# Optimization experiments

Hardware: AMD Instinct MI355X
Metric: run time of the kernel (lower is better)

The kernel has to match this reference:

```python
import jax, jax.numpy as jnp
import numpy as np

N = 100000   # n_entity
D = 128      # kg_emb_dim
R = 12       # n_relation
NB = 8       # num_bases
E = 1_000_000
P = 400_000  # hypergraph incidences
HE = 20_000  # hyperedges
B = 64       # users in batch
LR = 64      # related entities per hypergraph per user
LC = 32      # context entities per user
NH = 8       # mha heads
HD = D // NH


def setup_inputs() -> dict:
    key = jax.random.key(0)
    ks = jax.random.split(key, 32)
    s = 1.0 / np.sqrt(D)
    f = lambda i, shape, sc=s: jax.random.normal(ks[i], shape, dtype=jnp.float32) * sc
    ri = lambda i, shape, hi: jax.random.randint(ks[i], shape, 0, hi, dtype=jnp.int32)
    return {
        'entity_emb': f(0, (N, D)),
        'rgcn_bases': f(1, (NB, D, D)),
        'rgcn_comp': f(2, (R, NB)),
        'rgcn_root': f(3, (D, D)),
        'rgcn_bias': jnp.zeros((D,), jnp.float32),
        'sess_theta': f(4, (D, D)),
        'sess_bias': jnp.zeros((D,), jnp.float32),
        'know_theta': f(5, (D, D)),
        'know_bias': jnp.zeros((D,), jnp.float32),
        'in_proj_w': f(6, (3 * D, D)),
        'in_proj_b': jnp.zeros((3 * D,), jnp.float32),
        'out_proj_w': f(7, (D, D)),
        'out_proj_b': jnp.zeros((D,), jnp.float32),
        'attn_his_a': f(8, (D, D)),
        'attn_his_b': f(9, (D, 1)),
        'attn_a': f(10, (D, D)),
        'attn_b': f(11, (D, 1)),
        'rec_bias': jnp.zeros((N,), jnp.float32),
        'edge_src': ri(12, (E,), N),
        'edge_dst': ri(13, (E,), N),
        'edge_type': ri(14, (E,), R),
        'sess_nodes': ri(15, (P,), N),
        'sess_edges': ri(16, (P,), HE),
        'know_nodes': ri(17, (P,), N),
        'know_edges': ri(18, (P,), HE),
        'sess_rel_idx': ri(19, (B, LR), N),
        'know_rel_idx': ri(20, (B, LR), N),
        'context_idx': ri(21, (B, LC), N),
    }


def rgcn_conv(x, bases, comp, root, bias, src, dst, etype):
    # PyG RGCNConv with basis decomposition; per-relation mean aggregation
    # norm = 1/|N_r(i)| : count edges per (dst, relation)
    pair_key = dst * R + etype
    cnt = jax.ops.segment_sum(jnp.ones_like(src, dtype=x.dtype), pair_key, N * R)
    norm = 1.0 / jnp.maximum(cnt[pair_key], 1.0)  # [E]
    w = jnp.einsum('rb,bio->rio', comp, bases)    # [R, D, D]
    out = x @ root + bias
    for r in range(R):
        h_r = x @ w[r]                                            # [N, D]
        coef = norm * (etype == r).astype(x.dtype)                # [E]
        out = out + jax.ops.segment_sum(h_r[src] * coef[:, None], dst, N)
    return out


def hypergraph_conv(x, theta, bias, nodes, edges, n_hyperedges):
    # PyG HypergraphConv (no attention): D^-1 H W B^-1 H^T X Theta + bias
    xt = x @ theta                                                # [N, D]
    ones = jnp.ones(nodes.shape, x.dtype)
    b_deg = jax.ops.segment_sum(ones, edges, n_hyperedges)        # [HE]
    edge_feat = jax.ops.segment_sum(xt[nodes], edges, n_hyperedges)
    edge_feat = edge_feat * jnp.where(b_deg > 0, 1.0 / b_deg, 0.0)[:, None]
    d_deg = jax.ops.segment_sum(ones, nodes, N)                   # [N]
    out = jax.ops.segment_sum(edge_feat[edges], nodes, N)
    return out * jnp.where(d_deg > 0, 1.0 / d_deg, 0.0)[:, None] + bias


def self_attn_batch(h, a, b):
    # SelfAttentionBatch: e = tanh(h a) b; softmax over nodes; weighted sum
    e = jnp.einsum('bld,dk->blk', jnp.tanh(jnp.einsum('bld,de->ble', h, a)), b)[..., 0]
    attn = jax.nn.softmax(e, axis=-1)                             # [B, L]
    return jnp.einsum('bl,bld->bd', attn, h)


def mha(q, kv, in_proj_w, in_proj_b, out_proj_w, out_proj_b):
    # torch.nn.MultiheadAttention (batch_first) math
    wq, wk, wv = in_proj_w[:D], in_proj_w[D:2 * D], in_proj_w[2 * D:]
    bq, bk, bv = in_proj_b[:D], in_proj_b[D:2 * D], in_proj_b[2 * D:]
    qh = (q @ wq.T + bq).reshape(q.shape[0], q.shape[1], NH, HD)
    kh = (kv @ wk.T + bk).reshape(kv.shape[0], kv.shape[1], NH, HD)
    vh = (kv @ wv.T + bv).reshape(kv.shape[0], kv.shape[1], NH, HD)
    logits = jnp.einsum('bqhd,bkhd->bhqk', qh, kh) / np.sqrt(HD)
    attn = jax.nn.softmax(logits, axis=-1)
    o = jnp.einsum('bhqk,bkhd->bqhd', attn, vh).reshape(q.shape[0], q.shape[1], D)
    return o @ out_proj_w.T + out_proj_b


def reference(entity_emb, rgcn_bases, rgcn_comp, rgcn_root, rgcn_bias,
              sess_theta, sess_bias, know_theta, know_bias,
              in_proj_w, in_proj_b, out_proj_w, out_proj_b,
              attn_his_a, attn_his_b, attn_a, attn_b, rec_bias,
              edge_src, edge_dst, edge_type,
              sess_nodes, sess_edges, know_nodes, know_edges,
              sess_rel_idx, know_rel_idx, context_idx):
    # 1) RGCN over the full KG
    kg = rgcn_conv(entity_emb, rgcn_bases, rgcn_comp, rgcn_root, rgcn_bias,
                   edge_src, edge_dst, edge_type)
    # 2) session / knowledge hypergraph convolutions on RGCN output
    sess = hypergraph_conv(kg, sess_theta, sess_bias, sess_nodes, sess_edges, HE)
    know = hypergraph_conv(kg, know_theta, know_bias, know_nodes, know_edges, HE)
    # 3) per-user: related = concat(session_emb, knowledge_emb); context from kg
    related = jnp.concatenate([sess[sess_rel_idx], know[know_rel_idx]], axis=1)  # [B, 2LR, D]
    context = kg[context_idx]                                                    # [B, LC, D]
    # 4) MHItemAttention (context queries related) + gated attention pooling
    att_rel = mha(context, related, in_proj_w, in_proj_b, out_proj_w, out_proj_b)
    his = self_attn_batch(att_rel, attn_his_a, attn_his_b)                       # [B, D]
    user_cat = jnp.concatenate([context, his[:, None, :]], axis=1)               # [B, LC+1, D]
    user = self_attn_batch(user_cat, attn_a, attn_b)                             # [B, D]
    # 5) recommendation scores: F.linear(user, kg_embedding, rec_bias.bias)
    return user @ kg.T + rec_bias                                                # [B, N]
```

## Files before the change

kernel.cpp:

```cpp
#include <hip/hip_runtime.h>
#include <hip/hip_bf16.h>

#define DN 100000
#define DD 128
#define DR 12
#define DNB 8
#define DE 1000000
#define DP 400000
#define DHE 20000
#define DHE2 40000
#define DB 64
#define DLR 64
#define DLC 32
#define DNH 8
#define DHD 16
#define NRBINS (DR * DN)
#define SCAN_CHUNK 1024
#define MCAP 65536

typedef unsigned short ushortT;
typedef unsigned int uintT;
typedef __attribute__((ext_vector_type(8))) short s8v;
typedef __attribute__((ext_vector_type(4))) float f4v;

#define APAD 136

__device__ __forceinline__ ushortT rneb(float v) {
    uintT b = __float_as_uint(v);
    return (ushortT)((b + 0x7FFFu + ((b >> 16) & 1u)) >> 16);
}
__device__ __forceinline__ float b2f(ushortT h) {
    return __uint_as_float(((uintT)h) << 16);
}

__device__ __forceinline__ void split_store8(ushortT* hbase, ushortT* lbase, const float* v)
{
    ushortT h[8], l[8];
    #pragma unroll
    for (int j = 0; j < 8; ++j) {
        h[j] = rneb(v[j]);
        l[j] = rneb(v[j] - b2f(h[j]));
    }
    uint4 hv = make_uint4((uintT)h[0] | ((uintT)h[1] << 16), (uintT)h[2] | ((uintT)h[3] << 16),
                          (uintT)h[4] | ((uintT)h[5] << 16), (uintT)h[6] | ((uintT)h[7] << 16));
    uint4 lv = make_uint4((uintT)l[0] | ((uintT)l[1] << 16), (uintT)l[2] | ((uintT)l[3] << 16),
                          (uintT)l[4] | ((uintT)l[5] << 16), (uintT)l[6] | ((uintT)l[7] << 16));
    *(uint4*)hbase = hv;
    *(uint4*)lbase = lv;
}


__global__ __launch_bounds__(256) void k_presplit_all(
    const float* __restrict__ root, const float* __restrict__ st,
    const float* __restrict__ kt, const float* __restrict__ ipw,
    const float* __restrict__ opw, const float* __restrict__ aha,
    const float* __restrict__ aa, ushortT* __restrict__ outA)
{
    int gid = blockIdx.x * 256 + threadIdx.x;
    int mat = gid >> 14, e = gid & 16383;
    const float* srcs[9] = {root, st, kt, ipw, ipw + 16384, ipw + 32768, opw, aha, aa};
    const float* W = srcs[mat];
    bool t1 = (mat >= 3 && mat <= 6);
    int k = e & 31, n = (e >> 5) & 127, kc = e >> 12;
    float f = t1 ? W[(size_t)n * 128 + kc * 32 + k] : W[(size_t)(kc * 32 + k) * 128 + n];
    ushortT h = rneb(f);
    outA[(size_t)mat * 32768 + e] = h;
    outA[(size_t)mat * 32768 + 16384 + e] = rneb(f - b2f(h));
}

__global__ void k_wcomp_split(const float* __restrict__ comp, const float* __restrict__ bases,
                              ushortT* __restrict__ warena)
{
    int i = blockIdx.x * blockDim.x + threadIdx.x;
    if (i >= DR * DD * DD) return;
    int r = i / (DD * DD), io = i % (DD * DD);
    float s = 0.f;
    #pragma unroll
    for (int b = 0; b < DNB; ++b) s += comp[r * DNB + b] * bases[(size_t)b * DD * DD + io];
    int irow = io >> 7, o = io & 127;
    int kc = irow >> 5, k = irow & 31;
    size_t dst = (size_t)r * 32768 + (size_t)kc * 4096 + o * 32 + k;
    ushortT h = rneb(s);
    warena[dst] = h;
    warena[dst + 16384] = rneb(s - b2f(h));
}

__global__ __launch_bounds__(256) void k_gemm_ds(
    const float* __restrict__ A, const ushortT* __restrict__ Wb,
    const float* __restrict__ bias, const float* __restrict__ rs,
    float* __restrict__ C, int M)
{
    __shared__ __align__(16) ushortT Ah[64 * APAD], Al[64 * APAD];
    __shared__ __align__(16) ushortT Bs[8192];
    int tid = threadIdx.x;
    int row0 = blockIdx.x * 64;
    {
        int row = tid >> 2, c0 = (tid & 3) * 32;
        int gr = row0 + row;
        const float* ar = A + (size_t)gr * 128 + c0;
        float sc = 1.0f;
        if (rs && gr < M) { float d = rs[gr]; sc = (d > 0.f) ? 1.0f / d : 0.f; }
        #pragma unroll
        for (int g = 0; g < 4; ++g) {
            float v[8] = {};
            if (gr < M) {
                float4 u0 = *(const float4*)(ar + g * 8);
                float4 u1 = *(const float4*)(ar + g * 8 + 4);
                v[0]=u0.x*sc; v[1]=u0.y*sc; v[2]=u0.z*sc; v[3]=u0.w*sc;
                v[4]=u1.x*sc; v[5]=u1.y*sc; v[6]=u1.z*sc; v[7]=u1.w*sc;
            }
            split_store8(&Ah[row * APAD + c0 + g * 8], &Al[row * APAD + c0 + g * 8], v);
        }
    }
    f4v acc[8] = {};
    int w = tid >> 6, lane = tid & 63, m = lane & 15, quad = lane >> 4;
    for (int kc = 0; kc < 4; ++kc) {
        __syncthreads();
        {
            const ushortT* gh = Wb + kc * 4096;
            const ushortT* gl = Wb + 16384 + kc * 4096;
            *(s8v*)&Bs[tid * 8]        = *(const s8v*)&gh[tid * 8];
            *(s8v*)&Bs[2048 + tid * 8] = *(const s8v*)&gh[2048 + tid * 8];
            *(s8v*)&Bs[4096 + tid * 8] = *(const s8v*)&gl[tid * 8];
            *(s8v*)&Bs[6144 + tid * 8] = *(const s8v*)&gl[2048 + tid * 8];
        }
        __syncthreads();
        s8v ah = *(const s8v*)&Ah[(w * 16 + m) * APAD + kc * 32 + quad * 8];
        s8v al = *(const s8v*)&Al[(w * 16 + m) * APAD + kc * 32 + quad * 8];
        #pragma unroll
        for (int nt = 0; nt < 8; ++nt) {
            int boff = (nt * 16 + m) * 32 + quad * 8;
            s8v bh = *(const s8v*)&Bs[boff];
            s8v bl = *(const s8v*)&Bs[4096 + boff];
            acc[nt] = __builtin_amdgcn_mfma_f32_16x16x32_bf16(ah, bh, acc[nt], 0, 0, 0);
            acc[nt] = __builtin_amdgcn_mfma_f32_16x16x32_bf16(al, bh, acc[nt], 0, 0, 0);
            acc[nt] = __builtin_amdgcn_mfma_f32_16x16x32_bf16(ah, bl, acc[nt], 0, 0, 0);
        }
    }
    float bv[8];
    #pragma unroll
    for (int nt = 0; nt < 8; ++nt) bv[nt] = bias ? bias[nt * 16 + m] : 0.f;
    #pragma unroll
    for (int rr = 0; rr < 4; ++rr) {
        int gr = row0 + w * 16 + quad * 4 + rr;
        if (gr < M) {
            #pragma unroll
            for (int nt = 0; nt < 8; ++nt)
                C[(size_t)gr * 128 + nt * 16 + m] = acc[nt][rr] + bv[nt];
        }
    }
}

__global__ __launch_bounds__(256) void k_tanh_dot_ds(
    const float* __restrict__ A, const ushortT* __restrict__ Wb,
    const float* __restrict__ bvec, float* __restrict__ e, int M)
{
    __shared__ __align__(16) ushortT Ah[64 * APAD], Al[64 * APAD];
    __shared__ __align__(16) ushortT Bs[8192];
    int tid = threadIdx.x;
    int row0 = blockIdx.x * 64;
    {
        int row = tid >> 2, c0 = (tid & 3) * 32;
        int gr = row0 + row;
        const float* ar = A + (size_t)gr * 128 + c0;
        #pragma unroll
        for (int g = 0; g < 4; ++g) {
            float v[8] = {};
            if (gr < M) {
                float4 u0 = *(const float4*)(ar + g * 8);
                float4 u1 = *(const float4*)(ar + g * 8 + 4);
                v[0]=u0.x; v[1]=u0.y; v[2]=u0.z; v[3]=u0.w;
                v[4]=u1.x; v[5]=u1.y; v[6]=u1.z; v[7]=u1.w;
            }
            split_store8(&Ah[row * APAD + c0 + g * 8], &Al[row * APAD + c0 + g * 8], v);
        }
    }
    f4v acc[8] = {};
    int w = tid >> 6, lane = tid & 63, m = lane & 15, quad = lane >> 4;
    for (int kc = 0; kc < 4; ++kc) {
        __syncthreads();
        {
            const ushortT* gh = Wb + kc * 4096;
            const ushortT* gl = Wb + 16384 + kc * 4096;
            *(s8v*)&Bs[tid * 8]        = *(const s8v*)&gh[tid * 8];
            *(s8v*)&Bs[2048 + tid * 8] = *(const s8v*)&gh[2048 + tid * 8];
            *(s8v*)&Bs[4096 + tid * 8] = *(const s8v*)&gl[tid * 8];
            *(s8v*)&Bs[6144 + tid * 8] = *(const s8v*)&gl[2048 + tid * 8];
        }
        __syncthreads();
        s8v ah = *(const s8v*)&Ah[(w * 16 + m) * APAD + kc * 32 + quad * 8];
        s8v al = *(const s8v*)&Al[(w * 16 + m) * APAD + kc * 32 + quad * 8];
        #pragma unroll
        for (int nt = 0; nt < 8; ++nt) {
            int boff = (nt * 16 + m) * 32 + quad * 8;
            s8v bh = *(const s8v*)&Bs[boff];
            s8v bl = *(const s8v*)&Bs[4096 + boff];
            acc[nt] = __builtin_amdgcn_mfma_f32_16x16x32_bf16(ah, bh, acc[nt], 0, 0, 0);
            acc[nt] = __builtin_amdgcn_mfma_f32_16x16x32_bf16(al, bh, acc[nt], 0, 0, 0);
            acc[nt] = __builtin_amdgcn_mfma_f32_16x16x32_bf16(ah, bl, acc[nt], 0, 0, 0);
        }
    }
    float bv[8];
    #pragma unroll
    for (int nt = 0; nt < 8; ++nt) bv[nt] = bvec[nt * 16 + m];
    #pragma unroll
    for (int rr = 0; rr < 4; ++rr) {
        float p = 0.f;
        #pragma unroll
        for (int nt = 0; nt < 8; ++nt) p += tanhf(acc[nt][rr]) * bv[nt];
        #pragma unroll
        for (int o = 1; o < 16; o <<= 1) p += __shfl_xor(p, o);
        int gr = row0 + w * 16 + quad * 4 + rr;
        if (m == 0 && gr < M) e[gr] = p;
    }
}

template <int L>
__global__ __launch_bounds__(128) void k_pool_apply(const float* __restrict__ h,
                                                    const float* __restrict__ e,
                                                    float* __restrict__ out,
                                                    ushortT* __restrict__ us)
{
    __shared__ float es[L];
    int b = blockIdx.x, tid = threadIdx.x;
    if (tid < L) es[tid] = e[b * L + tid];
    __syncthreads();
    float mx = -1e30f;
    #pragma unroll
    for (int l = 0; l < L; ++l) mx = fmaxf(mx, es[l]);
    float wgt[L];
    float sum = 0.f;
    #pragma unroll
    for (int l = 0; l < L; ++l) { wgt[l] = __expf(es[l] - mx); sum += wgt[l]; }
    float inv = 1.0f / sum;
    float o = 0.f;
    #pragma unroll
    for (int l = 0; l < L; ++l) o += wgt[l] * h[((size_t)b * L + l) * 128 + tid];
    float val = o * inv;
    out[(size_t)b * 128 + tid] = val;
    if (us) {
        ushortT hh = rneb(val);
        ushortT ll = rneb(val - b2f(hh));
        int e_ = ((tid >> 5) * 2048) + b * 32 + (tid & 31);
        us[e_] = hh;
        us[8192 + e_] = ll;
    }
}

__global__ void k_build_ucat(const float* __restrict__ ctx, const float* __restrict__ his,
                             float* ucat)
{
    int i = blockIdx.x * blockDim.x + threadIdx.x;
    if (i >= DB * 33 * 128) return;
    int d = i & 127, l = (i >> 7) % 33, b = i / (33 * 128);
    ucat[i] = (l < 32) ? ctx[((size_t)b * 32 + l) * 128 + d] : his[(size_t)b * 128 + d];
}

__global__ __launch_bounds__(256) void k_rgcn_ds(
    const float* __restrict__ x, const ushortT* __restrict__ warena,
    const int* __restrict__ seglist, const int* __restrict__ soff,
    const int* __restrict__ slen, const int* __restrict__ ssrc,
    const int* __restrict__ stypebase, float* __restrict__ kg, int r)
{
    __shared__ __align__(16) ushortT Ah[64 * APAD], Al[64 * APAD];
    __shared__ __align__(16) ushortT Bs[8192];
    int s0 = stypebase[r], s1 = stypebase[r + 1];
    int base = s0 + blockIdx.x * 64;
    if (base >= s1) return;
    int nrow = min(64, s1 - base);
    int tid = threadIdx.x;
    const ushortT* Wb = warena + (size_t)r * 32768;
    {
        int row = tid >> 2, c0 = (tid & 3) * 32;
        float a[32] = {};
        if (row < nrow) {
            int key = seglist[base + row];
            int st = soff[key], len = slen[key];
            for (int i = 0; i < len; ++i) {
                const float* xr = x + (size_t)ssrc[st + i] * 128 + c0;
                #pragma unroll
                for (int j = 0; j < 8; ++j) {
                    float4 v = *(const float4*)(xr + j * 4);
                    a[j*4+0] += v.x; a[j*4+1] += v.y; a[j*4+2] += v.z; a[j*4+3] += v.w;
                }
            }
            float inv = 1.0f / (float)max(len, 1);
            #pragma unroll
            for (int j = 0; j < 32; ++j) a[j] *= inv;
        }
        #pragma unroll
        for (int g = 0; g < 4; ++g)
            split_store8(&Ah[row * APAD + c0 + g * 8], &Al[row * APAD + c0 + g * 8], a + g * 8);
    }
    f4v acc[8] = {};
    int w = tid >> 6, lane = tid & 63, m = lane & 15, quad = lane >> 4;
    for (int kc = 0; kc < 4; ++kc) {
        __syncthreads();
        {
            const ushortT* gh = Wb + kc * 4096;
            const ushortT* gl = Wb + 16384 + kc * 4096;
            *(s8v*)&Bs[tid * 8]        = *(const s8v*)&gh[tid * 8];
            *(s8v*)&Bs[2048 + tid * 8] = *(const s8v*)&gh[2048 + tid * 8];
            *(s8v*)&Bs[4096 + tid * 8] = *(const s8v*)&gl[tid * 8];
            *(s8v*)&Bs[6144 + tid * 8] = *(const s8v*)&gl[2048 + tid * 8];
        }
        __syncthreads();
        s8v ah = *(const s8v*)&Ah[(w * 16 + m) * APAD + kc * 32 + quad * 8];
        s8v al = *(const s8v*)&Al[(w * 16 + m) * APAD + kc * 32 + quad * 8];
        #pragma unroll
        for (int nt = 0; nt < 8; ++nt) {
            int boff = (nt * 16 + m) * 32 + quad * 8;
            s8v bh = *(const s8v*)&Bs[boff];
            s8v bl = *(const s8v*)&Bs[4096 + boff];
            acc[nt] = __builtin_amdgcn_mfma_f32_16x16x32_bf16(ah, bh, acc[nt], 0, 0, 0);
            acc[nt] = __builtin_amdgcn_mfma_f32_16x16x32_bf16(al, bh, acc[nt], 0, 0, 0);
            acc[nt] = __builtin_amdgcn_mfma_f32_16x16x32_bf16(ah, bl, acc[nt], 0, 0, 0);
        }
    }
    #pragma unroll
    for (int rr = 0; rr < 4; ++rr) {
        int rt = w * 16 + quad * 4 + rr;
        if (rt < nrow) {
            int dst = seglist[base + rt] - r * DN;
            float* kr = kg + (size_t)dst * 128 + m;
            #pragma unroll
            for (int nt = 0; nt < 8; ++nt)
                kr[nt * 16] += acc[nt][rr];
        }
    }
}

__global__ __launch_bounds__(256) void k_score_ds(
    const float* __restrict__ kg, const ushortT* __restrict__ Ub,
    const float* __restrict__ rb, float* __restrict__ out)
{
    __shared__ __align__(16) ushortT Ah[64 * APAD], Al[64 * APAD];
    __shared__ __align__(16) ushortT Bs[4096];
    int tid = threadIdx.x;
    int n0 = blockIdx.x * 64;
    {
        int row = tid >> 2, c0 = (tid & 3) * 32;
        int gr = n0 + row;
        const float* ar = kg + (size_t)gr * 128 + c0;
        #pragma unroll
        for (int g = 0; g < 4; ++g) {
            float v[8] = {};
            if (gr < DN) {
                float4 u0 = *(const float4*)(ar + g * 8);
                float4 u1 = *(const float4*)(ar + g * 8 + 4);
                v[0]=u0.x; v[1]=u0.y; v[2]=u0.z; v[3]=u0.w;
                v[4]=u1.x; v[5]=u1.y; v[6]=u1.z; v[7]=u1.w;
            }
            split_store8(&Ah[row * APAD + c0 + g * 8], &Al[row * APAD + c0 + g * 8], v);
        }
    }
    f4v acc[4] = {};
    int w = tid >> 6, lane = tid & 63, m = lane & 15, quad = lane >> 4;
    for (int kc = 0; kc < 4; ++kc) {
        __syncthreads();
        {
            const ushortT* gh = Ub + kc * 2048;
            const ushortT* gl = Ub + 8192 + kc * 2048;
            *(s8v*)&Bs[tid * 8]        = *(const s8v*)&gh[tid * 8];
            *(s8v*)&Bs[2048 + tid * 8] = *(const s8v*)&gl[tid * 8];
        }
        __syncthreads();
        s8v ah = *(const s8v*)&Ah[(w * 16 + m) * APAD + kc * 32 + quad * 8];
        s8v al = *(const s8v*)&Al[(w * 16 + m) * APAD + kc * 32 + quad * 8];
        #pragma unroll
        for (int nt = 0; nt < 4; ++nt) {
            int boff = (nt * 16 + m) * 32 + quad * 8;
            s8v bh = *(const s8v*)&Bs[boff];
            s8v bl = *(const s8v*)&Bs[2048 + boff];
            acc[nt] = __builtin_amdgcn_mfma_f32_16x16x32_bf16(ah, bh, acc[nt], 0, 0, 0);
            acc[nt] = __builtin_amdgcn_mfma_f32_16x16x32_bf16(al, bh, acc[nt], 0, 0, 0);
            acc[nt] = __builtin_amdgcn_mfma_f32_16x16x32_bf16(ah, bl, acc[nt], 0, 0, 0);
        }
    }
    int n = n0 + w * 16 + quad * 4;
    if (n < DN) {
        float4 rbv = *(const float4*)&rb[n];
        #pragma unroll
        for (int nt = 0; nt < 4; ++nt) {
            int b = nt * 16 + m;
            float4 o = make_float4(acc[nt][0] + rbv.x, acc[nt][1] + rbv.y,
                                   acc[nt][2] + rbv.z, acc[nt][3] + rbv.w);
            *(float4*)&out[(size_t)b * DN + n] = o;
        }
    }
}

__global__ void k_scan_pass1(const int* __restrict__ in, int n, int* __restrict__ bsum)
{
    __shared__ int red[256];
    int b = blockIdx.x, t = threadIdx.x;
    int i0 = b * SCAN_CHUNK + t * 4;
    int s = 0;
    #pragma unroll
    for (int j = 0; j < 4; ++j) {
        int i = i0 + j;
        if (i < n) s += in[i];
    }
    red[t] = s;
    __syncthreads();
    for (int o = 128; o > 0; o >>= 1) {
        if (t < o) red[t] += red[t + o];
        __syncthreads();
    }
    if (t == 0) bsum[b] = red[0];
}

__global__ __launch_bounds__(256) void k_scan_pass2p(int* bsum, int nb, int* total)
{
    __shared__ int lds[256];
    __shared__ int carry;
    int t = threadIdx.x;
    if (t == 0) carry = 0;
    __syncthreads();
    for (int c0 = 0; c0 < nb; c0 += 256) {
        int i = c0 + t;
        int v = (i < nb) ? bsum[i] : 0;
        lds[t] = v;
        __syncthreads();
        for (int o = 1; o < 256; o <<= 1) {
            int add = (t >= o) ? lds[t - o] : 0;
            __syncthreads();
            lds[t] += add;
            __syncthreads();
        }
        int myc = carry;
        if (i < nb) bsum[i] = lds[t] - v + myc;
        int tot = lds[255];
        __syncthreads();
        if (t == 0) carry = myc + tot;
        __syncthreads();
    }
    if (total && t == 0) *total = carry;
}

__global__ void k_scan_pass3(const int* __restrict__ in, int n, const int* __restrict__ bsum,
                             int* __restrict__ out)
{
    __shared__ int lds[256];
    int b = blockIdx.x, t = threadIdx.x;
    int i0 = b * SCAN_CHUNK + t * 4;
    int v[4]; int s = 0;
    #pragma unroll
    for (int j = 0; j < 4; ++j) {
        int i = i0 + j;
        int x = 0;
        if (i < n) x = in[i];
        v[j] = x; s += x;
    }
    lds[t] = s;
    __syncthreads();
    for (int o = 1; o < 256; o <<= 1) {
        int add = (t >= o) ? lds[t - o] : 0;
        __syncthreads();
        lds[t] += add;
        __syncthreads();
    }
    int run = lds[t] - s + bsum[b];
    #pragma unroll
    for (int j = 0; j < 4; ++j) {
        int i = i0 + j;
        if (i < n) { out[i] = run; run += v[j]; }
    }
}

__global__ void k_scan2_pass1(const int* __restrict__ in, int n, int* bV, int* bP)
{
    __shared__ int redV[256], redP[256];
    int b = blockIdx.x, t = threadIdx.x;
    int i0 = b * SCAN_CHUNK + t * 4;
    int sv = 0, sp = 0;
    #pragma unroll
    for (int j = 0; j < 4; ++j) {
        int i = i0 + j;
        if (i < n) { int v = in[i]; sv += v; sp += (v > 0); }
    }
    redV[t] = sv; redP[t] = sp;
    __syncthreads();
    for (int o = 128; o > 0; o >>= 1) {
        if (t < o) { redV[t] += redV[t + o]; redP[t] += redP[t + o]; }
        __syncthreads();
    }
    if (t == 0) { bV[b] = redV[0]; bP[b] = redP[0]; }
}

__global__ __launch_bounds__(256) void k_scan2_pass2(int* bV, int* bP, int nb, int* totalP)
{
    __shared__ int lds[256];
    __shared__ int carry;
    int t = threadIdx.x;
    #pragma unroll 1
    for (int which = 0; which < 2; ++which) {
        int* bsum = which ? bP : bV;
        __syncthreads();
        if (t == 0) carry = 0;
        __syncthreads();
        for (int c0 = 0; c0 < nb; c0 += 256) {
            int i = c0 + t;
            int v = (i < nb) ? bsum[i] : 0;
            lds[t] = v;
            __syncthreads();
            for (int o = 1; o < 256; o <<= 1) {
                int add = (t >= o) ? lds[t - o] : 0;
                __syncthreads();
                lds[t] += add;
                __syncthreads();
            }
            int myc = carry;
            if (i < nb) bsum[i] = lds[t] - v + myc;
            int tot = lds[255];
            __syncthreads();
            if (t == 0) carry = myc + tot;
            __syncthreads();
        }
        if (which == 1 && totalP && t == 0) *totalP = carry;
    }
}

__global__ void k_scan2_pass3(const int* __restrict__ in, int n,
                              const int* __restrict__ bV, const int* __restrict__ bP,
                              int* __restrict__ outV, int* __restrict__ outP)
{
    __shared__ int ldsV[256], ldsP[256];
    int b = blockIdx.x, t = threadIdx.x;
    int i0 = b * SCAN_CHUNK + t * 4;
    int v[4]; int sv = 0, sp = 0;
    #pragma unroll
    for (int j = 0; j < 4; ++j) {
        int i = i0 + j;
        int x = 0;
        if (i < n) x = in[i];
        v[j] = x; sv += x; sp += (x > 0);
    }
    ldsV[t] = sv; ldsP[t] = sp;
    __syncthreads();
    for (int o = 1; o < 256; o <<= 1) {
        int addV = (t >= o) ? ldsV[t - o] : 0;
        int addP = (t >= o) ? ldsP[t - o] : 0;
        __syncthreads();
        ldsV[t] += addV; ldsP[t] += addP;
        __syncthreads();
    }
    int runV = ldsV[t] - sv + bV[b];
    int runP = ldsP[t] - sp + bP[b];
    #pragma unroll
    for (int j = 0; j < 4; ++j) {
        int i = i0 + j;
        if (i < n) {
            outV[i] = runV; outP[i] = runP;
            runV += v[j]; runP += (v[j] > 0);
        }
    }
}

__global__ void k_hist_rgcn(const int* __restrict__ dst, const int* __restrict__ et,
                            int* hist, int E)
{
    int i = blockIdx.x * blockDim.x + threadIdx.x;
    if (i < E) atomicAdd(&hist[(size_t)et[i] * DN + dst[i]], 1);
}

__global__ void k_seglist(const int* __restrict__ hist, const int* __restrict__ segpos,
                          int* __restrict__ seglist, int n)
{
    int i = blockIdx.x * blockDim.x + threadIdx.x;
    if (i < n && hist[i] > 0) seglist[segpos[i]] = i;
}

__global__ void k_stypebase(const int* __restrict__ segpos, int* stypebase)
{
    int t = threadIdx.x;
    if (t < DR) stypebase[t] = segpos[(size_t)t * DN];
}

__global__ void k_bucket_rgcn(const int* __restrict__ src, const int* __restrict__ dst,
                              const int* __restrict__ et, const int* __restrict__ off,
                              int* cur, int* ssrc, int E)
{
    int i = blockIdx.x * blockDim.x + threadIdx.x;
    if (i >= E) return;
    int key = et[i] * DN + dst[i];
    int pos = off[key] + atomicAdd(&cur[key], 1);
    ssrc[pos] = src[i];
}

__global__ void k_hist_p2(const int* __restrict__ se, const int* __restrict__ ke, int* hist)
{
    int i = blockIdx.x * blockDim.x + threadIdx.x;
    if (i < DP) atomicAdd(&hist[se[i]], 1);
    else if (i < 2 * DP) atomicAdd(&hist[DHE + ke[i - DP]], 1);
}

__global__ void k_bucket_p2(const int* __restrict__ sn, const int* __restrict__ se,
                            const int* __restrict__ kn, const int* __restrict__ ke,
                            const int* __restrict__ off, int* cur, int* pns)
{
    int i = blockIdx.x * blockDim.x + threadIdx.x;
    if (i >= 2 * DP) return;
    int e, node;
    if (i < DP) { e = se[i]; node = sn[i]; }
    else { e = DHE + ke[i - DP]; node = kn[i - DP]; }
    int pos = off[e] + atomicAdd(&cur[e], 1);
    pns[pos] = node;
}

__global__ void k_hyper_agg(const float* __restrict__ xsrc, const int* __restrict__ pns,
                            const int* __restrict__ hoff, const int* __restrict__ hcnt,
                            const int* __restrict__ heneed, float* __restrict__ efeat)
{
    int lane = threadIdx.x & 63;
    int he = (blockIdx.x * blockDim.x + threadIdx.x) >> 6;
    if (he >= DHE2) return;
    if (!heneed[he]) return;
    int st = hoff[he], len = hcnt[he];
    int half = lane >> 5;
    int c16 = (lane & 31) * 4;
    float4 acc = make_float4(0.f, 0.f, 0.f, 0.f);
    int c = 0;
    for (; c + 4 <= len; c += 4) {
        int n0 = pns[st + c + half];
        int n1 = pns[st + c + 2 + half];
        float4 v0 = *(const float4*)&xsrc[(size_t)n0 * 128 + c16];
        float4 v1 = *(const float4*)&xsrc[(size_t)n1 * 128 + c16];
        acc.x += v0.x + v1.x; acc.y += v0.y + v1.y;
        acc.z += v0.z + v1.z; acc.w += v0.w + v1.w;
    }
    for (; c < len; c += 2) {
        int idx = c + half;
        if (idx < len) {
            int n = pns[st + idx];
            float4 v = *(const float4*)&xsrc[(size_t)n * 128 + c16];
            acc.x += v.x; acc.y += v.y; acc.z += v.z; acc.w += v.w;
        }
    }
    acc.x += __shfl_xor(acc.x, 32);
    acc.y += __shfl_xor(acc.y, 32);
    acc.z += __shfl_xor(acc.z, 32);
    acc.w += __shfl_xor(acc.w, 32);
    if (half == 0) {
        float inv = (len > 0) ? 1.0f / (float)len : 0.f;
        float4 o = make_float4(acc.x * inv, acc.y * inv, acc.z * inv, acc.w * inv);
        *(float4*)&efeat[(size_t)he * 128 + c16] = o;
    }
}

__global__ void k_slot_assign2(const int* __restrict__ sidx, const int* __restrict__ kidx,
                               int* slot_s, int* slot_k, int* scnt)
{
    int i = blockIdx.x * blockDim.x + threadIdx.x;
    if (i < DB * DLR) {
        int node = sidx[i];
        if (atomicCAS(&slot_s[node], -1, -2) == -1) slot_s[node] = atomicAdd(&scnt[0], 1);
    } else if (i < 2 * DB * DLR) {
        int node = kidx[i - DB * DLR];
        if (atomicCAS(&slot_k[node], -1, -2) == -1) slot_k[node] = atomicAdd(&scnt[1], 1);
    }
}

__global__ __launch_bounds__(256) void k_sdeg_match(
    const int* __restrict__ nodes, const int* __restrict__ he, const int* __restrict__ slot,
    float* sdeg, int* mcnt, int* mhe, int* msl, int* heneed, int heBase)
{
    __shared__ int lcnt, lbase;
    if (threadIdx.x == 0) lcnt = 0;
    __syncthreads();
    int i = blockIdx.x * 256 + threadIdx.x;
    int s = -1, lidx = 0, h = 0;
    if (i < DP) {
        s = slot[nodes[i]];
        if (s >= 0) {
            h = heBase + he[i];
            heneed[h] = 1;
            atomicAdd(&sdeg[s], 1.0f);
            lidx = atomicAdd(&lcnt, 1);
        }
    }
    __syncthreads();
    if (threadIdx.x == 0) lbase = (lcnt > 0) ? atomicAdd(mcnt, lcnt) : 0;
    __syncthreads();
    if (s >= 0) {
        int idx = lbase + lidx;
        if (idx < MCAP) { mhe[idx] = h; msl[idx] = s; }
    }
}

__global__ void k_accmatch2(const float* __restrict__ efeat,
                            const int* __restrict__ mhe_s, const int* __restrict__ msl_s,
                            const int* __restrict__ mhe_k, const int* __restrict__ msl_k,
                            const int* __restrict__ mcnt,
                            float* sacc_s, float* sacc_k)
{
    int lane = threadIdx.x & 63;
    int w = (blockIdx.x * blockDim.x + threadIdx.x) >> 6;
    int nw = (gridDim.x * blockDim.x) >> 6;
    int Ms = min(mcnt[0], MCAP), Mk = min(mcnt[1], MCAP);
    for (int i = w; i < Ms + Mk; i += nw) {
        bool sess = i < Ms;
        int he = sess ? mhe_s[i] : mhe_k[i - Ms];
        int sl = sess ? msl_s[i] : msl_k[i - Ms];
        float* sacc = sess ? sacc_s : sacc_k;
        float2 v = *(const float2*)&efeat[(size_t)he * 128 + lane * 2];
        atomicAdd(&sacc[(size_t)sl * 128 + lane * 2],     v.x);
        atomicAdd(&sacc[(size_t)sl * 128 + lane * 2 + 1], v.y);
    }
}

__global__ void k_rel_gather2(const float* __restrict__ so_s, const float* __restrict__ so_k,
                              const int* __restrict__ slot_s, const int* __restrict__ slot_k,
                              const int* __restrict__ ridx_s, const int* __restrict__ ridx_k,
                              float* __restrict__ related)
{
    int gid = blockIdx.x * blockDim.x + threadIdx.x;
    int i = gid >> 5, c = gid & 31;
    if (i >= 2 * DB * DLR) return;
    bool sess = i < DB * DLR;
    int ii = sess ? i : i - DB * DLR;
    int s = sess ? slot_s[ridx_s[ii]] : slot_k[ridx_k[ii]];
    const float* so = sess ? so_s : so_k;
    int b = ii / DLR, l = ii % DLR;
    int colOff = sess ? 0 : 64;
    ((float4*)&related[((size_t)b * 128 + colOff + l) * 128])[c] =
        ((const float4*)&so[(size_t)s * 128])[c];
}

__global__ void k_gather_rows(const float* __restrict__ src, const int* __restrict__ idx,
                              float* dst, int nRows)
{
    int i = blockIdx.x * blockDim.x + threadIdx.x;
    if (i >= nRows * 128) return;
    int row = i >> 7, d = i & 127;
    dst[i] = src[(size_t)idx[row] * 128 + d];
}

__global__ __launch_bounds__(256) void k_mha(const float* __restrict__ qb,
                                             const float* __restrict__ kb,
                                             const float* __restrict__ vb,
                                             float* __restrict__ ob)
{
    int b = blockIdx.x >> 3, h = blockIdx.x & 7;
    __shared__ float Ks[128][16], Vs[128][16], Qs[32][16];
    int tid = threadIdx.x;
    for (int i = tid; i < 128 * 16; i += 256) {
        int j = i >> 4, d = i & 15;
        Ks[j][d] = kb[((size_t)b * 128 + j) * 128 + h * 16 + d];
        Vs[j][d] = vb[((size_t)b * 128 + j) * 128 + h * 16 + d];
    }
    for (int i = tid; i < 32 * 16; i += 256) {
        int q = i >> 4, d = i & 15;
        Qs[q][d] = qb[((size_t)b * 32 + q) * 128 + h * 16 + d] * 0.25f;
    }
    __syncthreads();
    int q = tid >> 3;
    int jg = tid & 7;
    float lg[16];
    float m = -1e30f;
    #pragma unroll
    for (int jj = 0; jj < 16; ++jj) {
        int j = jg * 16 + jj;
        float s = 0.f;
        #pragma unroll
        for (int d = 0; d < 16; ++d) s += Qs[q][d] * Ks[j][d];
        lg[jj] = s;
        m = fmaxf(m, s);
    }
    #pragma unroll
    for (int o = 1; o < 8; o <<= 1) m = fmaxf(m, __shfl_xor(m, o));
    float sum = 0.f;
    float acc[16] = {};
    #pragma unroll
    for (int jj = 0; jj < 16; ++jj) {
        float p = __expf(lg[jj] - m);
        sum += p;
        int j = jg * 16 + jj;
        #pragma unroll
        for (int d = 0; d < 16; ++d) acc[d] += p * Vs[j][d];
    }
    #pragma unroll
    for (int o = 1; o < 8; o <<= 1) {
        sum += __shfl_xor(sum, o);
        #pragma unroll
        for (int d = 0; d < 16; ++d) acc[d] += __shfl_xor(acc[d], o);
    }
    if (jg == 0) {
        float inv = 1.0f / sum;
        #pragma unroll
        for (int d = 0; d < 16; ++d)
            ob[((size_t)b * 32 + q) * 128 + h * 16 + d] = acc[d] * inv;
    }
}

extern "C" void kernel_launch(void* const* d_in, const int* in_sizes, int n_in,
                              void* d_out, int out_size, void* d_ws, size_t ws_size,
                              hipStream_t stream)
{
    const float* emb        = (const float*)d_in[0];
    const float* bases      = (const float*)d_in[1];
    const float* comp       = (const float*)d_in[2];
    const float* root       = (const float*)d_in[3];
    const float* rgcn_bias  = (const float*)d_in[4];
    const float* sess_theta = (const float*)d_in[5];
    const float* sess_bias  = (const float*)d_in[6];
    const float* know_theta = (const float*)d_in[7];
    const float* know_bias  = (const float*)d_in[8];
    const float* in_proj_w  = (const float*)d_in[9];
    const float* in_proj_b  = (const float*)d_in[10];
    const float* out_proj_w = (const float*)d_in[11];
    const float* out_proj_b = (const float*)d_in[12];
    const float* attn_his_a = (const float*)d_in[13];
    const float* attn_his_b = (const float*)d_in[14];
    const float* attn_a     = (const float*)d_in[15];
    const float* attn_b     = (const float*)d_in[16];
    const float* rec_bias   = (const float*)d_in[17];
    const int* edge_src     = (const int*)d_in[18];
    const int* edge_dst     = (const int*)d_in[19];
    const int* edge_type    = (const int*)d_in[20];
    const int* sess_nodes   = (const int*)d_in[21];
    const int* sess_edges   = (const int*)d_in[22];
    const int* know_nodes   = (const int*)d_in[23];
    const int* know_edges   = (const int*)d_in[24];
    const int* sess_rel_idx = (const int*)d_in[25];
    const int* know_rel_idx = (const int*)d_in[26];
    const int* context_idx  = (const int*)d_in[27];
    float* out = (float*)d_out;

    float* wsf = (float*)d_ws;
    size_t off = 0;
    auto alloc = [&](size_t n) { size_t r = off; off += (n + 255) & ~(size_t)255; return r; };
    float* kg      = wsf + alloc(12800000);
    float* tmp     = wsf + alloc(12800000);
    ushortT* warena = (ushortT*)(wsf + alloc(196608));
    int*   bsumV   = (int*)(wsf + alloc(2048));
    int*   bsumP   = (int*)(wsf + alloc(2048));
    int*   stybase = (int*)(wsf + alloc(16));
    size_t zstart = off;
    int*   hhist   = (int*)(wsf + alloc(DHE2));
    int*   hcur    = (int*)(wsf + alloc(DHE2));
    int*   heneed  = (int*)(wsf + alloc(DHE2));
    int*   mcnt    = (int*)(wsf + alloc(16));
    int*   scnt    = (int*)(wsf + alloc(16));
    float* sdeg_s  = wsf + alloc(4096);
    float* sdeg_k  = wsf + alloc(4096);
    float* sacc_s  = wsf + alloc(524288);
    float* sacc_k  = wsf + alloc(524288);
    size_t zend = off;
    size_t fstart = off;
    int*   slot_s  = (int*)(wsf + alloc(100000));
    int*   slot_k  = (int*)(wsf + alloc(100000));
    size_t fend = off;
    int*   hoff    = (int*)(wsf + alloc(DHE2));
    int*   pns     = (int*)(wsf + alloc(2 * DP));
    int*   mhe_s   = (int*)(wsf + alloc(MCAP));
    int*   msl_s   = (int*)(wsf + alloc(MCAP));
    int*   mhe_k   = (int*)(wsf + alloc(MCAP));
    int*   msl_k   = (int*)(wsf + alloc(MCAP));
    float* so_s    = wsf + alloc(524288);
    float* so_k    = wsf + alloc(524288);
    float* related = wsf + alloc(1048576);
    float* ctx     = wsf + alloc(262144);
    float* qb      = wsf + alloc(262144);
    float* kb      = wsf + alloc(1048576);
    float* vb      = wsf + alloc(1048576);
    float* obuf    = wsf + alloc(262144);
    float* attrel  = wsf + alloc(262144);
    float* his     = wsf + alloc(8192);
    float* ucat    = wsf + alloc(270336);
    float* userb   = wsf + alloc(8192);
    float* e1      = wsf + alloc(2048);
    float* e2      = wsf + alloc(2112);
    (void)ws_size; (void)in_sizes; (void)n_in; (void)out_size;

    int*   hist    = (int*)tmp;
    int*   rcur    = (int*)tmp + 1200000;
    int*   soff    = (int*)tmp + 2400000;
    int*   segpos  = (int*)tmp + 3600000;
    int*   seglist = (int*)tmp + 4800000;
    int*   ssrc    = (int*)tmp + 6000000;
    float* efeat   = tmp + 7000000;
    ushortT* wsplit = (ushortT*)(tmp + 12200000);
    ushortT* usplit = (ushortT*)(tmp + 12400000);

    const int nbR = (NRBINS + SCAN_CHUNK - 1) / SCAN_CHUNK;
    const int nbH = (DHE2 + SCAN_CHUNK - 1) / SCAN_CHUNK;

    hipMemsetAsync(wsf + zstart, 0, (zend - zstart) * 4, stream);
    hipMemsetAsync(wsf + fstart, 0xFF, (fend - fstart) * 4, stream);
    hipMemsetAsync(hist, 0, 2400000 * 4, stream);

    k_presplit_all<<<576, 256, 0, stream>>>(root, sess_theta, know_theta, in_proj_w,
                                            out_proj_w, attn_his_a, attn_a, wsplit);

    k_slot_assign2<<<32, 256, 0, stream>>>(sess_rel_idx, know_rel_idx, slot_s, slot_k, scnt);
    k_sdeg_match<<<(DP + 255) / 256, 256, 0, stream>>>(sess_nodes, sess_edges, slot_s,
                                                       sdeg_s, mcnt, mhe_s, msl_s, heneed, 0);
    k_sdeg_match<<<(DP + 255) / 256, 256, 0, stream>>>(know_nodes, know_edges, slot_k,
                                                       sdeg_k, mcnt + 1, mhe_k, msl_k, heneed, DHE);

    k_hist_rgcn<<<(DE + 255) / 256, 256, 0, stream>>>(edge_dst, edge_type, hist, DE);
    k_scan2_pass1<<<nbR, 256, 0, stream>>>(hist, NRBINS, bsumV, bsumP);
    k_scan2_pass2<<<1, 256, 0, stream>>>(bsumV, bsumP, nbR, stybase + DR);
    k_scan2_pass3<<<nbR, 256, 0, stream>>>(hist, NRBINS, bsumV, bsumP, soff, segpos);
    k_stypebase<<<1, 64, 0, stream>>>(segpos, stybase);
    k_seglist<<<(NRBINS + 255) / 256, 256, 0, stream>>>(hist, segpos, seglist, NRBINS);
    k_bucket_rgcn<<<(DE + 255) / 256, 256, 0, stream>>>(edge_src, edge_dst, edge_type,
                                                        soff, rcur, ssrc, DE);
    k_wcomp_split<<<(DR * DD * DD + 255) / 256, 256, 0, stream>>>(comp, bases, warena);

    int gemmN = (DN + 63) / 64;
    k_gemm_ds<<<gemmN, 256, 0, stream>>>(emb, wsplit + 0 * 32768, rgcn_bias, nullptr, kg, DN);
    for (int r = 0; r < DR; ++r)
        k_rgcn_ds<<<gemmN, 256, 0, stream>>>(emb, warena, seglist, soff, hist, ssrc,
                                             stybase, kg, r);

    k_hist_p2<<<(2 * DP + 255) / 256, 256, 0, stream>>>(sess_edges, know_edges, hhist);
    k_scan_pass1<<<nbH, 256, 0, stream>>>(hhist, DHE2, bsumV);
    k_scan_pass2p<<<1, 256, 0, stream>>>(bsumV, nbH, nullptr);
    k_scan_pass3<<<nbH, 256, 0, stream>>>(hhist, DHE2, bsumV, hoff);
    k_bucket_p2<<<(2 * DP + 255) / 256, 256, 0, stream>>>(sess_nodes, sess_edges,
                                                          know_nodes, know_edges,
                                                          hoff, hcur, pns);
    k_hyper_agg<<<(DHE2 * 64 + 255) / 256, 256, 0, stream>>>(kg, pns, hoff, hhist, heneed, efeat);
    k_accmatch2<<<256, 256, 0, stream>>>(efeat, mhe_s, msl_s, mhe_k, msl_k, mcnt, sacc_s, sacc_k);

    k_gemm_ds<<<64, 256, 0, stream>>>(sacc_s, wsplit + 1 * 32768, sess_bias, sdeg_s, so_s, 4096);
    k_gemm_ds<<<64, 256, 0, stream>>>(sacc_k, wsplit + 2 * 32768, know_bias, sdeg_k, so_k, 4096);
    k_rel_gather2<<<(2 * DB * DLR * 32 + 255) / 256, 256, 0, stream>>>(
        so_s, so_k, slot_s, slot_k, sess_rel_idx, know_rel_idx, related);

    k_gather_rows<<<(DB * DLC * 128 + 255) / 256, 256, 0, stream>>>(kg, context_idx, ctx, DB * DLC);
    k_gemm_ds<<<(DB * DLC + 63) / 64, 256, 0, stream>>>(ctx, wsplit + 3 * 32768,
                                                        in_proj_b, nullptr, qb, DB * DLC);
    k_gemm_ds<<<(DB * 128 + 63) / 64, 256, 0, stream>>>(related, wsplit + 4 * 32768,
                                                        in_proj_b + DD, nullptr, kb, DB * 128);
    k_gemm_ds<<<(DB * 128 + 63) / 64, 256, 0, stream>>>(related, wsplit + 5 * 32768,
                                                        in_proj_b + 2 * DD, nullptr, vb, DB * 128);
    k_mha<<<DB * DNH, 256, 0, stream>>>(qb, kb, vb, obuf);
    k_gemm_ds<<<(DB * DLC + 63) / 64, 256, 0, stream>>>(obuf, wsplit + 6 * 32768,
                                                        out_proj_b, nullptr, attrel, DB * DLC);

    k_tanh_dot_ds<<<(DB * DLC + 63) / 64, 256, 0, stream>>>(attrel, wsplit + 7 * 32768,
                                                            attn_his_b, e1, DB * DLC);
    k_pool_apply<32><<<DB, 128, 0, stream>>>(attrel, e1, his, nullptr);
    k_build_ucat<<<(DB * 33 * 128 + 255) / 256, 256, 0, stream>>>(ctx, his, ucat);
    k_tanh_dot_ds<<<(DB * 33 + 63) / 64, 256, 0, stream>>>(ucat, wsplit + 8 * 32768,
                                                           attn_b, e2, DB * 33);
    k_pool_apply<33><<<DB, 128, 0, stream>>>(ucat, e2, userb, usplit);
    k_score_ds<<<gemmN, 256, 0, stream>>>(kg, usplit, rec_bias, out);
}
```

Baseline: 985.3 us.

## Merge per-relation RGCN launches into one kernel and fuse histogram/bucket passes

Replaces the 12 per-relation RGCN launches, each sized for all nodes with most blocks exiting early, with a single launch. A prefix table maps each block to its relation, and because blocks from different relations may now hit the same destination row concurrently, the output update becomes an atomicAdd. The RGCN and hypergraph histogram and bucketing kernels are merged. Bucketing now increments the scan offsets in place, which removes the cursor arrays, and readers subtract the length to recover the segment start. The context row gather is folded into the Q-projection GEMM, which also writes the gathered rows out. The cost is float atomics on kg, which make the summation order nondeterministic.

```diff
diff --git a/kernel.cpp b/kernel.cpp
--- a/kernel.cpp
+++ b/kernel.cpp
@@ -49,7 +49,6 @@
     *(uint4*)lbase = lv;
 }
 
-
 __global__ __launch_bounds__(256) void k_presplit_all(
     const float* __restrict__ root, const float* __restrict__ st,
     const float* __restrict__ kt, const float* __restrict__ ipw,
@@ -88,6 +87,7 @@
 __global__ __launch_bounds__(256) void k_gemm_ds(
     const float* __restrict__ A, const ushortT* __restrict__ Wb,
     const float* __restrict__ bias, const float* __restrict__ rs,
+    const int* __restrict__ gidx, float* __restrict__ gout,
     float* __restrict__ C, int M)
 {
     __shared__ __align__(16) ushortT Ah[64 * APAD], Al[64 * APAD];
@@ -97,7 +97,9 @@
     {
         int row = tid >> 2, c0 = (tid & 3) * 32;
         int gr = row0 + row;
-        const float* ar = A + (size_t)gr * 128 + c0;
+        int arow = gr;
+        if (gidx && gr < M) arow = gidx[gr];
+        const float* ar = A + (size_t)arow * 128 + c0;
         float sc = 1.0f;
         if (rs && gr < M) { float d = rs[gr]; sc = (d > 0.f) ? 1.0f / d : 0.f; }
         #pragma unroll
@@ -108,6 +110,10 @@
                 float4 u1 = *(const float4*)(ar + g * 8 + 4);
                 v[0]=u0.x*sc; v[1]=u0.y*sc; v[2]=u0.z*sc; v[3]=u0.w*sc;
                 v[4]=u1.x*sc; v[5]=u1.y*sc; v[6]=u1.z*sc; v[7]=u1.w*sc;
+                if (gout) {
+                    *(float4*)(gout + (size_t)gr * 128 + c0 + g * 8)     = u0;
+                    *(float4*)(gout + (size_t)gr * 128 + c0 + g * 8 + 4) = u1;
+                }
             }
             split_store8(&Ah[row * APAD + c0 + g * 8], &Al[row * APAD + c0 + g * 8], v);
         }
@@ -256,17 +262,22 @@
     ucat[i] = (l < 32) ? ctx[((size_t)b * 32 + l) * 128 + d] : his[(size_t)b * 128 + d];
 }
 
-__global__ __launch_bounds__(256) void k_rgcn_ds(
+__global__ __launch_bounds__(256) void k_rgcn_all(
     const float* __restrict__ x, const ushortT* __restrict__ warena,
     const int* __restrict__ seglist, const int* __restrict__ soff,
     const int* __restrict__ slen, const int* __restrict__ ssrc,
-    const int* __restrict__ stypebase, float* __restrict__ kg, int r)
+    const int* __restrict__ stypebase, const int* __restrict__ bo,
+    float* __restrict__ kg)
 {
     __shared__ __align__(16) ushortT Ah[64 * APAD], Al[64 * APAD];
     __shared__ __align__(16) ushortT Bs[8192];
+    int bid = blockIdx.x;
+    if (bid >= bo[DR]) return;
+    int r = 0;
+    #pragma unroll 1
+    while (bid >= bo[r + 1]) ++r;
     int s0 = stypebase[r], s1 = stypebase[r + 1];
-    int base = s0 + blockIdx.x * 64;
-    if (base >= s1) return;
+    int base = s0 + (bid - bo[r]) * 64;
     int nrow = min(64, s1 - base);
     int tid = threadIdx.x;
     const ushortT* Wb = warena + (size_t)r * 32768;
@@ -275,7 +286,8 @@
         float a[32] = {};
         if (row < nrow) {
             int key = seglist[base + row];
-            int st = soff[key], len = slen[key];
+            int len = slen[key];
+            int st = soff[key] - len;
             for (int i = 0; i < len; ++i) {
                 const float* xr = x + (size_t)ssrc[st + i] * 128 + c0;
                 #pragma unroll
@@ -325,7 +337,7 @@
             float* kr = kg + (size_t)dst * 128 + m;
             #pragma unroll
             for (int nt = 0; nt < 8; ++nt)
-                kr[nt * 16] += acc[nt][rr];
+                atomicAdd(&kr[nt * 16], acc[nt][rr]);
         }
     }
 }
@@ -557,11 +569,19 @@
     }
 }
 
-__global__ void k_hist_rgcn(const int* __restrict__ dst, const int* __restrict__ et,
-                            int* hist, int E)
+__global__ void k_hist_both(const int* __restrict__ dst, const int* __restrict__ et,
+                            int* __restrict__ hist,
+                            const int* __restrict__ se, const int* __restrict__ ke,
+                            int* __restrict__ hhist)
 {
     int i = blockIdx.x * blockDim.x + threadIdx.x;
-    if (i < E) atomicAdd(&hist[(size_t)et[i] * DN + dst[i]], 1);
+    if (i < DE) {
+        atomicAdd(&hist[(size_t)et[i] * DN + dst[i]], 1);
+    } else {
+        int j = i - DE;
+        if (j < DP) atomicAdd(&hhist[se[j]], 1);
+        else if (j < 2 * DP) atomicAdd(&hhist[DHE + ke[j - DP]], 1);
+    }
 }
 
 __global__ void k_seglist(const int* __restrict__ hist, const int* __restrict__ segpos,
@@ -571,41 +591,43 @@
     if (i < n && hist[i] > 0) seglist[segpos[i]] = i;
 }
 
-__global__ void k_stypebase(const int* __restrict__ segpos, int* stypebase)
+__global__ void k_stypebase(const int* __restrict__ segpos, int* stybase, int* bo)
 {
     int t = threadIdx.x;
-    if (t < DR) stypebase[t] = segpos[(size_t)t * DN];
-}
-
-__global__ void k_bucket_rgcn(const int* __restrict__ src, const int* __restrict__ dst,
-                              const int* __restrict__ et, const int* __restrict__ off,
-                              int* cur, int* ssrc, int E)
+    if (t < DR) stybase[t] = segpos[(size_t)t * DN];
+    if (t == 0) {
+        int acc = 0; bo[0] = 0;
+        int prev = segpos[0];
+        for (int r = 0; r < DR; ++r) {
+            int nxt = (r == DR - 1) ? stybase[DR] : segpos[(size_t)(r + 1) * DN];
+            acc += (nxt - prev + 63) >> 6;
+            bo[r + 1] = acc;
+            prev = nxt;
+        }
+    }
+}
+
+__global__ void k_bucket_both(const int* __restrict__ src, const int* __restrict__ dst,
+                              const int* __restrict__ et, int* __restrict__ soff,
+                              int* __restrict__ ssrc,
+                              const int* __restrict__ sn, const int* __restrict__ se,
+                              const int* __restrict__ kn, const int* __restrict__ ke,
+                              int* __restrict__ hoff, int* __restrict__ pns)
 {
     int i = blockIdx.x * blockDim.x + threadIdx.x;
-    if (i >= E) return;
-    int key = et[i] * DN + dst[i];
-    int pos = off[key] + atomicAdd(&cur[key], 1);
-    ssrc[pos] = src[i];
-}
-
-__global__ void k_hist_p2(const int* __restrict__ se, const int* __restrict__ ke, int* hist)
-{
-    int i = blockIdx.x * blockDim.x + threadIdx.x;
-    if (i < DP) atomicAdd(&hist[se[i]], 1);
-    else if (i < 2 * DP) atomicAdd(&hist[DHE + ke[i - DP]], 1);
-}
-
-__global__ void k_bucket_p2(const int* __restrict__ sn, const int* __restrict__ se,
-                            const int* __restrict__ kn, const int* __restrict__ ke,
-                            const int* __restrict__ off, int* cur, int* pns)
-{
-    int i = blockIdx.x * blockDim.x + threadIdx.x;
-    if (i >= 2 * DP) return;
-    int e, node;
-    if (i < DP) { e = se[i]; node = sn[i]; }
-    else { e = DHE + ke[i - DP]; node = kn[i - DP]; }
-    int pos = off[e] + atomicAdd(&cur[e], 1);
-    pns[pos] = node;
+    if (i < DE) {
+        int key = et[i] * DN + dst[i];
+        int pos = atomicAdd(&soff[key], 1);
+        ssrc[pos] = src[i];
+    } else {
+        int j = i - DE;
+        if (j >= 2 * DP) return;
+        int e, node;
+        if (j < DP) { e = se[j]; node = sn[j]; }
+        else { e = DHE + ke[j - DP]; node = kn[j - DP]; }
+        int pos = atomicAdd(&hoff[e], 1);
+        pns[pos] = node;
+    }
 }
 
 __global__ void k_hyper_agg(const float* __restrict__ xsrc, const int* __restrict__ pns,
@@ -616,7 +638,8 @@
     int he = (blockIdx.x * blockDim.x + threadIdx.x) >> 6;
     if (he >= DHE2) return;
     if (!heneed[he]) return;
-    int st = hoff[he], len = hcnt[he];
+    int len = hcnt[he];
+    int st = hoff[he] - len;
     int half = lane >> 5;
     int c16 = (lane & 31) * 4;
     float4 acc = make_float4(0.f, 0.f, 0.f, 0.f);
@@ -725,15 +748,6 @@
     int colOff = sess ? 0 : 64;
     ((float4*)&related[((size_t)b * 128 + colOff + l) * 128])[c] =
         ((const float4*)&so[(size_t)s * 128])[c];
-}
-
-__global__ void k_gather_rows(const float* __restrict__ src, const int* __restrict__ idx,
-                              float* dst, int nRows)
-{
-    int i = blockIdx.x * blockDim.x + threadIdx.x;
-    if (i >= nRows * 128) return;
-    int row = i >> 7, d = i & 127;
-    dst[i] = src[(size_t)idx[row] * 128 + d];
 }
 
 __global__ __launch_bounds__(256) void k_mha(const float* __restrict__ qb,
@@ -836,9 +850,9 @@
     int*   bsumV   = (int*)(wsf + alloc(2048));
     int*   bsumP   = (int*)(wsf + alloc(2048));
     int*   stybase = (int*)(wsf + alloc(16));
+    int*   bo      = (int*)(wsf + alloc(16));
     size_t zstart = off;
     int*   hhist   = (int*)(wsf + alloc(DHE2));
-    int*   hcur    = (int*)(wsf + alloc(DHE2));
     int*   heneed  = (int*)(wsf + alloc(DHE2));
     int*   mcnt    = (int*)(wsf + alloc(16));
     int*   scnt    = (int*)(wsf + alloc(16));
@@ -874,12 +888,11 @@
     (void)ws_size; (void)in_sizes; (void)n_in; (void)out_size;
 
     int*   hist    = (int*)tmp;
-    int*   rcur    = (int*)tmp + 1200000;
-    int*   soff    = (int*)tmp + 2400000;
-    int*   segpos  = (int*)tmp + 3600000;
-    int*   seglist = (int*)tmp + 4800000;
-    int*   ssrc    = (int*)tmp + 6000000;
-    float* efeat   = tmp + 7000000;
+    int*   soff    = (int*)tmp + 1200000;
+    int*   segpos  = (int*)tmp + 2400000;
+    int*   seglist = (int*)tmp + 3600000;
+    int*   ssrc    = (int*)tmp + 4800000;
+    float* efeat   = tmp + 6000000;
     ushortT* wsplit = (ushortT*)(tmp + 12200000);
     ushortT* usplit = (ushortT*)(tmp + 12400000);
 
@@ -888,7 +901,7 @@
 
     hipMemsetAsync(wsf + zstart, 0, (zend - zstart) * 4, stream);
     hipMemsetAsync(wsf + fstart, 0xFF, (fend - fstart) * 4, stream);
-    hipMemsetAsync(hist, 0, 2400000 * 4, stream);
+    hipMemsetAsync(hist, 0, (size_t)NRBINS * 4, stream);
 
     k_presplit_all<<<576, 256, 0, stream>>>(root, sess_theta, know_theta, in_proj_w,
                                             out_proj_w, attn_his_a, attn_a, wsplit);
@@ -899,47 +912,53 @@
     k_sdeg_match<<<(DP + 255) / 256, 256, 0, stream>>>(know_nodes, know_edges, slot_k,
                                                        sdeg_k, mcnt + 1, mhe_k, msl_k, heneed, DHE);
 
-    k_hist_rgcn<<<(DE + 255) / 256, 256, 0, stream>>>(edge_dst, edge_type, hist, DE);
+    k_hist_both<<<(DE + 2 * DP + 255) / 256, 256, 0, stream>>>(edge_dst, edge_type, hist,
+                                                               sess_edges, know_edges, hhist);
     k_scan2_pass1<<<nbR, 256, 0, stream>>>(hist, NRBINS, bsumV, bsumP);
     k_scan2_pass2<<<1, 256, 0, stream>>>(bsumV, bsumP, nbR, stybase + DR);
     k_scan2_pass3<<<nbR, 256, 0, stream>>>(hist, NRBINS, bsumV, bsumP, soff, segpos);
-    k_stypebase<<<1, 64, 0, stream>>>(segpos, stybase);
-    k_seglist<<<(NRBINS + 255) / 256, 256, 0, stream>>>(hist, segpos, seglist, NRBINS);
-    k_bucket_rgcn<<<(DE + 255) / 256, 256, 0, stream>>>(edge_src, edge_dst, edge_type,
-                                                        soff, rcur, ssrc, DE);
-    k_wcomp_split<<<(DR * DD * DD + 255) / 256, 256, 0, stream>>>(comp, bases, warena);
-
-    int gemmN = (DN + 63) / 64;
-    k_gemm_ds<<<gemmN, 256, 0, stream>>>(emb, wsplit + 0 * 32768, rgcn_bias, nullptr, kg, DN);
-    for (int r = 0; r < DR; ++r)
-        k_rgcn_ds<<<gemmN, 256, 0, stream>>>(emb, warena, seglist, soff, hist, ssrc,
-                                             stybase, kg, r);
-
-    k_hist_p2<<<(2 * DP + 255) / 256, 256, 0, stream>>>(sess_edges, know_edges, hhist);
     k_scan_pass1<<<nbH, 256, 0, stream>>>(hhist, DHE2, bsumV);
     k_scan_pass2p<<<1, 256, 0, stream>>>(bsumV, nbH, nullptr);
     k_scan_pass3<<<nbH, 256, 0, stream>>>(hhist, DHE2, bsumV, hoff);
-    k_bucket_p2<<<(2 * DP + 255) / 256, 256, 0, stream>>>(sess_nodes, sess_edges,
-                                                          know_nodes, know_edges,
-                                                          hoff, hcur, pns);
+
+    k_stypebase<<<1, 64, 0, stream>>>(segpos, stybase, bo);
+    k_seglist<<<(NRBINS + 255) / 256, 256, 0, stream>>>(hist, segpos, seglist, NRBINS);
+
+    k_bucket_both<<<(DE + 2 * DP + 255) / 256, 256, 0, stream>>>(
+        edge_src, edge_dst, edge_type, soff, ssrc,
+        sess_nodes, sess_edges, know_nodes, know_edges, hoff, pns);
+
+    k_wcomp_split<<<(DR * DD * DD + 255) / 256, 256, 0, stream>>>(comp, bases, warena);
+
+    int gemmN = (DN + 63) / 64;
+    k_gemm_ds<<<gemmN, 256, 0, stream>>>(emb, wsplit + 0 * 32768, rgcn_bias, nullptr,
+                                         nullptr, nullptr, kg, DN);
+    k_rgcn_all<<<(DE + 63) / 64 + DR, 256, 0, stream>>>(emb, warena, seglist, soff, hist,
+                                                        ssrc, stybase, bo, kg);
+
     k_hyper_agg<<<(DHE2 * 64 + 255) / 256, 256, 0, stream>>>(kg, pns, hoff, hhist, heneed, efeat);
     k_accmatch2<<<256, 256, 0, stream>>>(efeat, mhe_s, msl_s, mhe_k, msl_k, mcnt, sacc_s, sacc_k);
 
-    k_gemm_ds<<<64, 256, 0, stream>>>(sacc_s, wsplit + 1 * 32768, sess_bias, sdeg_s, so_s, 4096);
-    k_gemm_ds<<<64, 256, 0, stream>>>(sacc_k, wsplit + 2 * 32768, know_bias, sdeg_k, so_k, 4096);
+    k_gemm_ds<<<64, 256, 0, stream>>>(sacc_s, wsplit + 1 * 32768, sess_bias, sdeg_s,
+                                      nullptr, nullptr, so_s, 4096);
+    k_gemm_ds<<<64, 256, 0, stream>>>(sacc_k, wsplit + 2 * 32768, know_bias, sdeg_k,
+                                      nullptr, nullptr, so_k, 4096);
     k_rel_gather2<<<(2 * DB * DLR * 32 + 255) / 256, 256, 0, stream>>>(
         so_s, so_k, slot_s, slot_k, sess_rel_idx, know_rel_idx, related);
 
-    k_gather_rows<<<(DB * DLC * 128 + 255) / 256, 256, 0, stream>>>(kg, context_idx, ctx, DB * DLC);
-    k_gemm_ds<<<(DB * DLC + 63) / 64, 256, 0, stream>>>(ctx, wsplit + 3 * 32768,
-                                                        in_proj_b, nullptr, qb, DB * DLC);
+    k_gemm_ds<<<(DB * DLC + 63) / 64, 256, 0, stream>>>(kg, wsplit + 3 * 32768,
+                                                        in_proj_b, nullptr,
+                                                        context_idx, ctx, qb, DB * DLC);
     k_gemm_ds<<<(DB * 128 + 63) / 64, 256, 0, stream>>>(related, wsplit + 4 * 32768,
-                                                        in_proj_b + DD, nullptr, kb, DB * 128);
+                                                        in_proj_b + DD, nullptr,
+                                                        nullptr, nullptr, kb, DB * 128);
     k_gemm_ds<<<(DB * 128 + 63) / 64, 256, 0, stream>>>(related, wsplit + 5 * 32768,
-                                                        in_proj_b + 2 * DD, nullptr, vb, DB * 128);
+                                                        in_proj_b + 2 * DD, nullptr,
+                                                        nullptr, nullptr, vb, DB * 128);
     k_mha<<<DB * DNH, 256, 0, stream>>>(qb, kb, vb, obuf);
     k_gemm_ds<<<(DB * DLC + 63) / 64, 256, 0, stream>>>(obuf, wsplit + 6 * 32768,
-                                                        out_proj_b, nullptr, attrel, DB * DLC);
+                                                        out_proj_b, nullptr,
+                                                        nullptr, nullptr, attrel, DB * DLC);
 
     k_tanh_dot_ds<<<(DB * DLC + 63) / 64, 256, 0, stream>>>(attrel, wsplit + 7 * 32768,
                                                             attn_his_b, e1, DB * DLC);
```

New measurement: 968.1 us. Within noise of the previous version (-1.8%).
